# Optimization experiments

Hardware: AMD Instinct MI355X
Metric: run time of the kernel (lower is better)

## Reference

```python
import jax, jax.numpy as jnp
import numpy as np

UNITS = 512
MEMORY_SIZE = 16


def setup_inputs() -> dict:
    key = jax.random.key(0)
    k1, k2, k3, k4, k5 = jax.random.split(key, 5)
    B, T, D = 256, 128, 512
    inputs = jax.random.normal(k1, (B, T, D), dtype=jnp.float32)
    dones = jax.random.randint(k2, (B, T), 0, 2, dtype=jnp.int32)
    state = jnp.zeros((B, UNITS), dtype=jnp.float32)
    step = jnp.zeros((B, 1), dtype=jnp.int32)
    # GRU params (Keras default reset_after=True: dual bias [2, 3*units])
    W = jax.random.normal(k3, (D, 3 * UNITS), dtype=jnp.float32) * 0.05
    U = jax.random.normal(k4, (UNITS, 3 * UNITS), dtype=jnp.float32) * 0.05
    b = jax.random.normal(k5, (2, 3 * UNITS), dtype=jnp.float32) * 0.05
    return {"inputs": inputs, "dones": dones, "state": state, "step": step,
            "W": W, "U": U, "b": b}


def _gru_cell(h, x, W, U, b):
    # Keras GRU, reset_after=True
    xm = x @ W + b[0]          # [B, 3U]
    hm = h @ U + b[1]          # [B, 3U]
    xz, xr, xh = jnp.split(xm, 3, axis=-1)
    hz, hr, hh = jnp.split(hm, 3, axis=-1)
    z = jax.nn.sigmoid(xz + hz)
    r = jax.nn.sigmoid(xr + hr)
    hcand = jnp.tanh(xh + r * hh)
    return z * h + (1.0 - z) * hcand


def reference(inputs, dones, state, step, W, U, b):
    # inputs: [B, T, D]; dones: [B, T]; state: [B, U]; step: [B, 1] int32
    x_t = jnp.transpose(inputs, (1, 0, 2))  # [T, B, D]
    d_t = jnp.transpose(dones, (1, 0))      # [T, B]

    def scan_fn(carry, xs):
        h, s = carry
        x, d = xs
        h_new = _gru_cell(h, x, W, U, b)
        s_new = s + 1
        reset = (d == 1) | ((s_new[:, 0] % MEMORY_SIZE) == 0)  # [B]
        h_out = jnp.where(reset[:, None], 0.0, h_new)
        s_out = jnp.where(reset[:, None], 0, s_new)
        # hidden_state emitted per step is the cell output BEFORE reset masking
        return (h_out, s_out), h_new

    (state_f, step_f), seq = jax.lax.scan(scan_fn, (state, step), (x_t, d_t))
    sequences = jnp.transpose(seq, (1, 0, 2))  # [B, T, U]
    return sequences, state_f, step_f
```

## Files before the change

kernel.cpp:

```cpp
#include <hip/hip_runtime.h>
#include <cstdint>

#define UNITS 512
#define NB 256
#define NT 128
#define ND 512
#define G3 1536

#define SEQ_ELEMS (16777216L)
#define STATE_OFF (SEQ_ELEMS)
#define STEP_OFF  (SEQ_ELEMS + 131072L)

#define ROWS_PER_BG 16

#define WS_FLAG_OFF 4096
#define WS_H_OFF    65536
#define H_ELEMS     131072L

typedef unsigned short u16;
typedef short short8 __attribute__((ext_vector_type(8)));
typedef float f32x4 __attribute__((ext_vector_type(4)));
typedef unsigned int u32;

__device__ __forceinline__ u16 f2b(float f) {
  u32 x = __float_as_uint(f);
  u32 r = (x + 0x7FFFu + ((x >> 16) & 1u)) >> 16;
  return (u16)r;
}
__device__ __forceinline__ float b2f(u16 u) {
  return __uint_as_float(((u32)u) << 16);
}

template<int MODE>
__device__ __forceinline__ float ldf(const void* p, long idx) {
  if (MODE) return b2f(((const u16*)p)[idx]);
  else      return ((const float*)p)[idx];
}

__device__ __forceinline__ void store_h_coherent(const u16* p, u16 v) {
  u32 vv = v;
  asm volatile("global_store_short %0, %1, off sc0 sc1"
               :: "v"(p), "v"(vv) : "memory");
}
__device__ __forceinline__ void st_flag(const u32* p, u32 v) {
  asm volatile("global_store_dword %0, %1, off sc0 sc1"
               :: "v"(p), "v"(v) : "memory");
}
__device__ __forceinline__ u32 load_flag_coherent(const u32* p) {
  u32 v;
  asm volatile("global_load_dword %0, %1, off sc0 sc1\n\t"
               "s_waitcnt vmcnt(0)"
               : "=v"(v) : "v"(p) : "memory");
  return v;
}

__device__ __forceinline__ void load_h16_coherent(const u16* p, short8 hf[16]) {
  asm volatile(
    "global_load_dwordx4 %0, %16, off sc0 sc1\n\t"
    "global_load_dwordx4 %1, %16, off offset:64 sc0 sc1\n\t"
    "global_load_dwordx4 %2, %16, off offset:128 sc0 sc1\n\t"
    "global_load_dwordx4 %3, %16, off offset:192 sc0 sc1\n\t"
    "global_load_dwordx4 %4, %16, off offset:256 sc0 sc1\n\t"
    "global_load_dwordx4 %5, %16, off offset:320 sc0 sc1\n\t"
    "global_load_dwordx4 %6, %16, off offset:384 sc0 sc1\n\t"
    "global_load_dwordx4 %7, %16, off offset:448 sc0 sc1\n\t"
    "global_load_dwordx4 %8, %16, off offset:512 sc0 sc1\n\t"
    "global_load_dwordx4 %9, %16, off offset:576 sc0 sc1\n\t"
    "global_load_dwordx4 %10, %16, off offset:640 sc0 sc1\n\t"
    "global_load_dwordx4 %11, %16, off offset:704 sc0 sc1\n\t"
    "global_load_dwordx4 %12, %16, off offset:768 sc0 sc1\n\t"
    "global_load_dwordx4 %13, %16, off offset:832 sc0 sc1\n\t"
    "global_load_dwordx4 %14, %16, off offset:896 sc0 sc1\n\t"
    "global_load_dwordx4 %15, %16, off offset:960 sc0 sc1\n\t"
    "s_waitcnt vmcnt(0)"
    : "=&v"(hf[0]), "=&v"(hf[1]), "=&v"(hf[2]), "=&v"(hf[3]),
      "=&v"(hf[4]), "=&v"(hf[5]), "=&v"(hf[6]), "=&v"(hf[7]),
      "=&v"(hf[8]), "=&v"(hf[9]), "=&v"(hf[10]), "=&v"(hf[11]),
      "=&v"(hf[12]), "=&v"(hf[13]), "=&v"(hf[14]), "=&v"(hf[15])
    : "v"(p)
    : "memory");
}

__global__ void sniff_init(const void* W, u32* wsu) {
  int l = threadIdx.x;
  u32 v = ((const u32*)W)[l];
  u32 elo = (v >> 7) & 0xFFu;
  bool inband = (elo > 90u) && (elo < 130u);
  unsigned long long m = __ballot(inband);
  int cnt = __popcll(m);
  if (l == 0) wsu[0] = (cnt >= 32) ? 1u : 0u;
}

__global__ void h_init(const void* state, void* ws) {
  u32 flag = *(const u32*)ws;
  u16* h0 = (u16*)((char*)ws + WS_H_OFF);
  int i = blockIdx.x * blockDim.x + threadIdx.x;
  if (i < (int)H_ELEMS) {
    h0[i] = flag ? ((const u16*)state)[i] : f2b(((const float*)state)[i]);
  }
  if (i < 8192) {
    ((u32*)((char*)ws + WS_FLAG_OFF))[i] = 0u;
  }
}

template<int MODE>
__device__ void stage_cols(const void* M, int ug, u16* lds) {
  int tid = threadIdx.x;
  #pragma unroll 4
  for (int it = 0; it < 192; ++it) {
    int idx = it * 256 + tid;
    int k = idx / 96;
    int c = idx - k * 96;
    int col = (c >> 5) * UNITS + ug * 32 + (c & 31);
    float v = ldf<MODE>(M, (long)k * G3 + col);
    u32 byte = (u32)c * 1024u +
               ((((u32)k) * 2u) ^ (((u32)(c & 7)) << 4));
    *(u16*)((char*)lds + byte) = f2b(v);
  }
}

__device__ __forceinline__ short8 read_bfrag(const u16* lds, int c, int k) {
  u32 byte = (u32)c * 1024u +
             ((((u32)k) * 2u) ^ (((u32)(c & 7)) << 4));
  return *(const short8*)((const char*)lds + byte);
}

#define MFMA(a, b, c) __builtin_amdgcn_mfma_f32_16x16x32_bf16((a), (b), (c), 0, 0, 0)

template<int MODE>
__global__ __launch_bounds__(256, 1)
void gru_run(const void* __restrict__ xin, const int* __restrict__ dones,
             const int* __restrict__ stepin, const void* __restrict__ stin,
             const void* __restrict__ W,
             const void* __restrict__ U, const void* __restrict__ bias,
             void* __restrict__ out, void* __restrict__ ws)
{
  u32 flag = *(const u32*)ws;
  if (flag != (u32)MODE) return;

  __shared__ u16  wl[96 * 512];
  __shared__ float xmbuf[4][2][3][64][4];
  __shared__ int   dlds[16][NT];
  __shared__ u32   sv[8];

  const int tid  = threadIdx.x;
  const int wv   = tid >> 6;
  const int l    = tid & 63;
  const int l15  = l & 15;
  const int ksub = (l >> 4) * 8;
  const int rsub = (l >> 4) * 4;

  const int bg = blockIdx.x & 15;
  const int ug = blockIdx.x >> 4;
  const int r0 = bg * ROWS_PER_BG;

  u32* flags = (u32*)((char*)ws + WS_FLAG_OFF);
  u16* hws = (u16*)((char*)ws + WS_H_OFF);

  if (tid < 8) sv[tid] = 0u;
  #pragma unroll
  for (int q = 0; q < 8; ++q) {
    int idx = q * 256 + tid;
    dlds[idx >> 7][idx & 127] = dones[(long)(r0 + (idx >> 7)) * NT + (idx & 127)];
  }

  stage_cols<MODE>(U, ug, wl);
  __syncthreads();
  short8 ufz[16], ufrr[16], ufh[16];
  if (wv < 2) {
    #pragma unroll
    for (int kt = 0; kt < 16; ++kt) {
      int kb = kt * 32 + ksub;
      ufz[kt]  = read_bfrag(wl,      wv * 16 + l15, kb);
      ufrr[kt] = read_bfrag(wl, 32 + wv * 16 + l15, kb);
      ufh[kt]  = read_bfrag(wl, 64 + wv * 16 + l15, kb);
    }
  }
  __syncthreads();
  stage_cols<MODE>(W, ug, wl);
  __syncthreads();

  if (wv >= 2) {
    const int xw = wv - 2;
    const int c0 = xw * 16 + l15, c1 = 32 + xw * 16 + l15, c2 = 64 + xw * 16 + l15;
    for (int t = 0; t < NT; ++t) {
      const int p = t & 3;
      const u32 u = (u32)(t >> 2);
      long xbase = ((long)(r0 + l15) * NT + t) * ND + ksub;
      short8 xf[16];
      #pragma unroll
      for (int kt = 0; kt < 16; ++kt) {
        if (MODE) {
          xf[kt] = *(const short8*)((const u16*)xin + xbase + kt * 32);
        } else {
          const float* q = (const float*)xin + xbase + kt * 32;
          f32x4 lo = *(const f32x4*)q;
          f32x4 hi = *(const f32x4*)(q + 4);
          short8 r;
          r[0] = (short)f2b(lo[0]); r[1] = (short)f2b(lo[1]);
          r[2] = (short)f2b(lo[2]); r[3] = (short)f2b(lo[3]);
          r[4] = (short)f2b(hi[0]); r[5] = (short)f2b(hi[1]);
          r[6] = (short)f2b(hi[2]); r[7] = (short)f2b(hi[3]);
          xf[kt] = r;
        }
      }
      if (u > 0) {
        while (__hip_atomic_load(&sv[4 + p], __ATOMIC_ACQUIRE,
                                 __HIP_MEMORY_SCOPE_WORKGROUP) < 2u * u) {}
      }
      f32x4 az = {0,0,0,0}, ar = {0,0,0,0}, axh = {0,0,0,0};
      #pragma unroll
      for (int kt = 0; kt < 16; ++kt) {
        int kb = kt * 32 + ksub;
        az  = MFMA(xf[kt], read_bfrag(wl, c0, kb), az);
        ar  = MFMA(xf[kt], read_bfrag(wl, c1, kb), ar);
        axh = MFMA(xf[kt], read_bfrag(wl, c2, kb), axh);
      }
      *(f32x4*)&xmbuf[p][xw][0][l][0] = az;
      *(f32x4*)&xmbuf[p][xw][1][l][0] = ar;
      *(f32x4*)&xmbuf[p][xw][2][l][0] = axh;
      __hip_atomic_fetch_add(&sv[p], (l == 0) ? 1u : 0u, __ATOMIC_RELEASE,
                             __HIP_MEMORY_SCOPE_WORKGROUP);
    }
    return;
  }

  const int w = wv;
  const int j = ug * 32 + w * 16 + l15;
  u32* myflag = flags + (long)(bg * 32 + ug * 2 + w) * 16;

  float bzs = ldf<MODE>(bias, j)        + ldf<MODE>(bias, G3 + j);
  float brs = ldf<MODE>(bias, 512 + j)  + ldf<MODE>(bias, G3 + 512 + j);
  float bxh = ldf<MODE>(bias, 1024 + j);
  float bhh = ldf<MODE>(bias, (long)G3 + 1024 + j);

  int sarr[4];
  float hprev[4];
  #pragma unroll
  for (int i = 0; i < 4; ++i) {
    int row = r0 + rsub + i;
    sarr[i]  = stepin[row];
    hprev[i] = ldf<MODE>(stin, (long)row * UNITS + j);
  }

  const long hbase = (long)(r0 + l15) * UNITS + ksub;

  for (int t = 0; t < NT; ++t) {
    const int p = t & 3;
    const u32 u = (u32)(t >> 2);

    if (t > 0) {
      const u32* fp_ = flags + (long)(bg * 32 + l) * 16;
      bool pred;
      do {
        u32 fv = (l < 32) ? load_flag_coherent(fp_) : (u32)t;
        pred = (fv >= (u32)t);
      } while (!__all(pred));
    }

    const u16* hb = hws + (long)(t & 1) * H_ELEMS;
    short8 hf[16];
    load_h16_coherent(hb + hbase, hf);

    f32x4 az = {0,0,0,0}, ar = {0,0,0,0}, ahh = {0,0,0,0};
    #pragma unroll
    for (int kt = 0; kt < 16; ++kt) {
      az  = MFMA(hf[kt], ufz[kt],  az);
      ar  = MFMA(hf[kt], ufrr[kt], ar);
      ahh = MFMA(hf[kt], ufh[kt],  ahh);
    }

    while (__hip_atomic_load(&sv[p], __ATOMIC_ACQUIRE,
                             __HIP_MEMORY_SCOPE_WORKGROUP) < 2u * (u + 1u)) {}
    f32x4 axh = *(const f32x4*)&xmbuf[p][w][2][l][0];
    {
      f32x4 xz = *(const f32x4*)&xmbuf[p][w][0][l][0];
      f32x4 xr = *(const f32x4*)&xmbuf[p][w][1][l][0];
      az[0] += xz[0]; az[1] += xz[1]; az[2] += xz[2]; az[3] += xz[3];
      ar[0] += xr[0]; ar[1] += xr[1]; ar[2] += xr[2]; ar[3] += xr[3];
    }
    __hip_atomic_fetch_add(&sv[4 + p], (l == 0) ? 1u : 0u, __ATOMIC_RELEASE,
                           __HIP_MEMORY_SCOPE_WORKGROUP);

    u16* hn = hws + (long)((t + 1) & 1) * H_ELEMS;
    float hnew_r[4];
    #pragma unroll
    for (int i = 0; i < 4; ++i) {
      int row = r0 + rsub + i;
      float z  = 1.0f / (1.0f + __expf(-(az[i] + bzs)));
      float rr = 1.0f / (1.0f + __expf(-(ar[i] + brs)));
      float tx = axh[i] + bxh + rr * (ahh[i] + bhh);
      tx = fminf(15.0f, fmaxf(-15.0f, tx));
      float e  = __expf(2.0f * tx);
      float hcand = (e - 1.0f) / (e + 1.0f);
      float hnew = z * hprev[i] + (1.0f - z) * hcand;
      hnew_r[i] = hnew;

      int sn = sarr[i] + 1;
      bool reset = (dlds[rsub + i][t] == 1) || ((sn & 15) == 0);
      float hkeep = reset ? 0.0f : hnew;
      sarr[i] = reset ? 0 : sn;
      hprev[i] = hkeep;
      if (t < NT - 1)
        store_h_coherent(hn + (long)row * UNITS + j, f2b(hkeep));
    }

    if (t < NT - 1) {
      asm volatile("s_waitcnt vmcnt(0)" ::: "memory");
      if (l == 0) st_flag(myflag, (u32)(t + 1));
    }

    #pragma unroll
    for (int i = 0; i < 4; ++i) {
      int row = r0 + rsub + i;
      long qo = ((long)row * NT + t) * UNITS + j;
      if (MODE) ((u16*)out)[qo] = f2b(hnew_r[i]);
      else      ((float*)out)[qo] = hnew_r[i];

      if (t == NT - 1) {
        long so = STATE_OFF + (long)row * UNITS + j;
        if (MODE) ((u16*)out)[so] = f2b(hprev[i]);
        else      ((float*)out)[so] = hprev[i];
        if (w == 0 && l15 == 0 && ug == 0) {
          long po = STEP_OFF + row;
          float sval = (float)sarr[i];
          if (MODE) ((u16*)out)[po] = f2b(sval);
          else      ((float*)out)[po] = sval;
        }
      }
    }
  }
}

extern "C" void kernel_launch(void* const* d_in, const int* in_sizes, int n_in,
                              void* d_out, int out_size, void* d_ws, size_t ws_size,
                              hipStream_t stream) {
  const void* xin    = d_in[0];
  const int*  dones  = (const int*)d_in[1];
  const void* stin   = d_in[2];
  const int*  stepin = (const int*)d_in[3];
  const void* W      = d_in[4];
  const void* U      = d_in[5];
  const void* bias   = d_in[6];

  sniff_init<<<1, 64, 0, stream>>>(W, (u32*)d_ws);
  h_init<<<256, 512, 0, stream>>>(stin, d_ws);
  gru_run<0><<<256, 256, 0, stream>>>(xin, dones, stepin, stin, W, U, bias, d_out, d_ws);
  gru_run<1><<<256, 256, 0, stream>>>(xin, dones, stepin, stin, W, U, bias, d_out, d_ws);
}
```

Measured before the change: 838.8 us.

## Stage hidden-state tile in LDS and publish with 16-byte stores, one flag per block

Each block now collects its 16x32 slice of the new hidden state in shared memory. One wave then writes it to the global exchange buffer with coalesced 16-byte coherent stores, replacing scattered 2-byte stores from both waves. The per-step readiness flags drop from two per block (one per wave) to one, so consumers poll 16 flags instead of 32. The change adds an intra-block LDS barrier before publishing, and the sequence-output stores now happen before the publish rather than after it.

```diff
diff --git a/kernel.cpp b/kernel.cpp
--- a/kernel.cpp
+++ b/kernel.cpp
@@ -21,6 +21,7 @@
 typedef short short8 __attribute__((ext_vector_type(8)));
 typedef float f32x4 __attribute__((ext_vector_type(4)));
 typedef unsigned int u32;
+typedef unsigned int u32x4 __attribute__((ext_vector_type(4)));
 
 __device__ __forceinline__ u16 f2b(float f) {
   u32 x = __float_as_uint(f);
@@ -37,10 +38,9 @@
   else      return ((const float*)p)[idx];
 }
 
-__device__ __forceinline__ void store_h_coherent(const u16* p, u16 v) {
-  u32 vv = v;
-  asm volatile("global_store_short %0, %1, off sc0 sc1"
-               :: "v"(p), "v"(vv) : "memory");
+__device__ __forceinline__ void st_h16B(const u32x4* p, u32x4 v) {
+  asm volatile("global_store_dwordx4 %0, %1, off sc0 sc1"
+               :: "v"(p), "v"(v) : "memory");
 }
 __device__ __forceinline__ void st_flag(const u32* p, u32 v) {
   asm volatile("global_store_dword %0, %1, off sc0 sc1"
@@ -98,8 +98,8 @@
   if (i < (int)H_ELEMS) {
     h0[i] = flag ? ((const u16*)state)[i] : f2b(((const float*)state)[i]);
   }
-  if (i < 8192) {
-    ((u32*)((char*)ws + WS_FLAG_OFF))[i] = 0u;
+  if (i < 4096) {
+    st_flag(((u32*)((char*)ws + WS_FLAG_OFF)) + i, 0u);
   }
 }
 
@@ -141,7 +141,8 @@
   __shared__ u16  wl[96 * 512];
   __shared__ float xmbuf[4][2][3][64][4];
   __shared__ int   dlds[16][NT];
-  __shared__ u32   sv[8];
+  __shared__ u16   gtile[16][32];
+  __shared__ u32   sv[12];
 
   const int tid  = threadIdx.x;
   const int wv   = tid >> 6;
@@ -157,7 +158,7 @@
   u32* flags = (u32*)((char*)ws + WS_FLAG_OFF);
   u16* hws = (u16*)((char*)ws + WS_H_OFF);
 
-  if (tid < 8) sv[tid] = 0u;
+  if (tid < 12) sv[tid] = 0u;
   #pragma unroll
   for (int q = 0; q < 8; ++q) {
     int idx = q * 256 + tid;
@@ -227,7 +228,7 @@
 
   const int w = wv;
   const int j = ug * 32 + w * 16 + l15;
-  u32* myflag = flags + (long)(bg * 32 + ug * 2 + w) * 16;
+  u32* myflag = flags + (long)(bg * 16 + ug) * 16;
 
   float bzs = ldf<MODE>(bias, j)        + ldf<MODE>(bias, G3 + j);
   float brs = ldf<MODE>(bias, 512 + j)  + ldf<MODE>(bias, G3 + 512 + j);
@@ -244,16 +245,18 @@
   }
 
   const long hbase = (long)(r0 + l15) * UNITS + ksub;
+  const int prow = l >> 2;
+  const long pbyte_row = (long)(r0 + prow) * UNITS + ug * 32 + (l & 3) * 8;
 
   for (int t = 0; t < NT; ++t) {
     const int p = t & 3;
     const u32 u = (u32)(t >> 2);
 
     if (t > 0) {
-      const u32* fp_ = flags + (long)(bg * 32 + l) * 16;
+      const u32* fp_ = flags + (long)(bg * 16 + l15) * 16;
       bool pred;
       do {
-        u32 fv = (l < 32) ? load_flag_coherent(fp_) : (u32)t;
+        u32 fv = (l < 16) ? load_flag_coherent(fp_) : (u32)t;
         pred = (fv >= (u32)t);
       } while (!__all(pred));
     }
@@ -282,8 +285,6 @@
     __hip_atomic_fetch_add(&sv[4 + p], (l == 0) ? 1u : 0u, __ATOMIC_RELEASE,
                            __HIP_MEMORY_SCOPE_WORKGROUP);
 
-    u16* hn = hws + (long)((t + 1) & 1) * H_ELEMS;
-    float hnew_r[4];
     #pragma unroll
     for (int i = 0; i < 4; ++i) {
       int row = r0 + rsub + i;
@@ -294,40 +295,46 @@
       float e  = __expf(2.0f * tx);
       float hcand = (e - 1.0f) / (e + 1.0f);
       float hnew = z * hprev[i] + (1.0f - z) * hcand;
-      hnew_r[i] = hnew;
 
       int sn = sarr[i] + 1;
       bool reset = (dlds[rsub + i][t] == 1) || ((sn & 15) == 0);
       float hkeep = reset ? 0.0f : hnew;
       sarr[i] = reset ? 0 : sn;
       hprev[i] = hkeep;
-      if (t < NT - 1)
-        store_h_coherent(hn + (long)row * UNITS + j, f2b(hkeep));
+      gtile[rsub + i][w * 16 + l15] = f2b(hkeep);
+
+      long qo = ((long)row * NT + t) * UNITS + j;
+      if (MODE) ((u16*)out)[qo] = f2b(hnew);
+      else      ((float*)out)[qo] = hnew;
     }
 
     if (t < NT - 1) {
-      asm volatile("s_waitcnt vmcnt(0)" ::: "memory");
-      if (l == 0) st_flag(myflag, (u32)(t + 1));
-    }
-
-    #pragma unroll
-    for (int i = 0; i < 4; ++i) {
-      int row = r0 + rsub + i;
-      long qo = ((long)row * NT + t) * UNITS + j;
-      if (MODE) ((u16*)out)[qo] = f2b(hnew_r[i]);
-      else      ((float*)out)[qo] = hnew_r[i];
-
-      if (t == NT - 1) {
-        long so = STATE_OFF + (long)row * UNITS + j;
-        if (MODE) ((u16*)out)[so] = f2b(hprev[i]);
-        else      ((float*)out)[so] = hprev[i];
-        if (w == 0 && l15 == 0 && ug == 0) {
-          long po = STEP_OFF + row;
-          float sval = (float)sarr[i];
-          if (MODE) ((u16*)out)[po] = f2b(sval);
-          else      ((float*)out)[po] = sval;
-        }
+      asm volatile("s_waitcnt lgkmcnt(0)" ::: "memory");
+      __hip_atomic_fetch_add(&sv[8], (l == 0) ? 1u : 0u, __ATOMIC_RELEASE,
+                             __HIP_MEMORY_SCOPE_WORKGROUP);
+      while (__hip_atomic_load(&sv[8], __ATOMIC_ACQUIRE,
+                               __HIP_MEMORY_SCOPE_WORKGROUP) < 2u * (u32)(t + 1)) {}
+      if (w == 0) {
+        u16* hn = hws + (long)((t + 1) & 1) * H_ELEMS;
+        u32x4 pv = *(const u32x4*)&gtile[prow][(l & 3) * 8];
+        st_h16B((const u32x4*)(hn + pbyte_row), pv);
+        asm volatile("s_waitcnt vmcnt(0)" ::: "memory");
+        if (l == 0) st_flag(myflag, (u32)(t + 1));
       }
+    }
+  }
+
+  #pragma unroll
+  for (int i = 0; i < 4; ++i) {
+    int row = r0 + rsub + i;
+    long so = STATE_OFF + (long)row * UNITS + j;
+    if (MODE) ((u16*)out)[so] = f2b(hprev[i]);
+    else      ((float*)out)[so] = hprev[i];
+    if (w == 0 && l15 == 0 && ug == 0) {
+      long po = STEP_OFF + row;
+      float sval = (float)sarr[i];
+      if (MODE) ((u16*)out)[po] = f2b(sval);
+      else      ((float*)out)[po] = sval;
     }
   }
 }
```

Result: slower. 921.6 us (+9.9%).
